# Optimization experiments

Hardware: AMD Instinct MI355X
Metric: run time of the kernel (lower is better)

The kernel has to match this reference:

```python
import jax, jax.numpy as jnp
import numpy as np
from jax import lax


def setup_inputs() -> dict:
    key = jax.random.key(0)
    k1, k2 = jax.random.split(key)
    B, H, W, Cin, Cout, kh, kw = 16, 128, 128, 128, 128, 3, 3
    X = jax.random.normal(k1, (B, H, W, Cin), dtype=jnp.float32)
    kernel = jax.random.normal(k2, (B, kh, kw, Cin, Cout), dtype=jnp.float32) * 0.05
    return {"X": X, "kernel": kernel}


def _conv_one(x, k):
    # x: [H, W, Cin]; k: [kh, kw, Cin, Cout] -> [H', W', Cout]
    out = lax.conv_general_dilated(
        x[None],  # [1, H, W, Cin]
        k,
        window_strides=(1, 1),
        padding='VALID',
        dimension_numbers=('NHWC', 'HWIO', 'NHWC'),
    )
    return out[0]


def reference(X, kernel):
    # Per-sample dynamic-filter conv: each batch element convolved with its own
    # [kh, kw, Cin, Cout] filter. Equivalent to the TF depthwise-reshape trick
    # followed by reduce_sum over the input-channel axis.
    return jax.vmap(_conv_one)(X, kernel)  # [B, H', W', Cout]
```

## Files before the change

### kernel.cpp

```cpp
#include <hip/hip_runtime.h>
#include <cstdint>

#define OWD 126
#define MTOT 15876

typedef short bf16x8 __attribute__((ext_vector_type(8)));
typedef float f32x4  __attribute__((ext_vector_type(4)));

#define BT_ELEMS  (16u * 128u * 1152u)
#define XBF_ELEMS (16u * 128u * 128u * 128u)
#define WS_NEEDED ((size_t)(BT_ELEMS + XBF_ELEMS) * 2)

__device__ __forceinline__ uint16_t f2bf(float f) {
    union { float f; uint32_t u; } v;
    v.f = f;
    uint32_t u = v.u;
    return (uint16_t)((u + 0x7FFFu + ((u >> 16) & 1u)) >> 16);
}

__device__ __forceinline__ uint32_t pk2(float a, float b) {
    return (uint32_t)f2bf(a) | ((uint32_t)f2bf(b) << 16);
}

__device__ __forceinline__ void gl_lds16(const uint16_t* g, uint16_t* l) {
    __builtin_amdgcn_global_load_lds(
        (const __attribute__((address_space(1))) uint32_t*)g,
        (__attribute__((address_space(3))) uint32_t*)l, 16, 0, 0);
}

__global__ __launch_bounds__(256) void kprep(const float* __restrict__ Kin,
                                             uint16_t* __restrict__ Bt) {
    const int rs = blockIdx.x;
    const int b  = blockIdx.y;
    const int t  = threadIdx.x;
    const int n  = t & 127;
    const int og = t >> 7;

    const float* src = Kin + (((size_t)b * 9 + rs) << 14);
    uint16_t*    dst = Bt + ((size_t)b * 128 + n) * 1152 + rs * 128;

#pragma unroll
    for (int o = 0; o < 8; ++o) {
        const int oct = og * 8 + o;
        const float* s0 = src + (oct * 8) * 128 + n;
        uint4 p;
        p.x = pk2(s0[0 * 128], s0[1 * 128]);
        p.y = pk2(s0[2 * 128], s0[3 * 128]);
        p.z = pk2(s0[4 * 128], s0[5 * 128]);
        p.w = pk2(s0[6 * 128], s0[7 * 128]);
        *(uint4*)(dst + oct * 8) = p;
    }
}

__global__ __launch_bounds__(256) void xprep(const float* __restrict__ X,
                                             uint16_t* __restrict__ Xbf) {
    const size_t i = ((size_t)blockIdx.x * 256 + threadIdx.x) * 8;
    const float4 a = *(const float4*)(X + i);
    const float4 b = *(const float4*)(X + i + 4);
    uint4 p;
    p.x = pk2(a.x, a.y);
    p.y = pk2(a.z, a.w);
    p.z = pk2(b.x, b.y);
    p.w = pk2(b.z, b.w);
    *(uint4*)(Xbf + i) = p;
}

__global__ __launch_bounds__(256) void conv_mfma_a(const uint16_t* __restrict__ Xbf,
                                                   const uint16_t* __restrict__ Bt,
                                                   float* __restrict__ Out) {
    __shared__ __align__(16) uint16_t lA[128 * 64];
    __shared__ __align__(16) uint16_t lB[128 * 64];

    const int mtile = blockIdx.x;
    const int b     = blockIdx.y;
    const int tid   = threadIdx.x;
    const int lane  = tid & 63;
    const int wave  = tid >> 6;
    const int wm    = (wave & 1) << 6;
    const int wn    = (wave >> 1) << 6;
    const int l15   = lane & 15;
    const int quad  = lane >> 4;

    const int kc = (lane & 7) ^ (lane >> 3);
    const uint16_t* Asrc[4];
    const uint16_t* Bsrc[4];
#pragma unroll
    for (int i = 0; i < 4; ++i) {
        const int row = wave * 32 + i * 8 + (lane >> 3);
        int m = mtile * 128 + row;
        if (m >= MTOT) m = MTOT - 1;
        const int oh = m / OWD, ow = m - oh * OWD;
        Asrc[i] = Xbf + (((size_t)b * 128 + oh) * 128 + ow) * 128 + kc * 8;
        Bsrc[i] = Bt + ((size_t)b * 128 + row) * 1152 + kc * 8;
    }
    uint16_t* Adst = &lA[(wave * 256 + lane) * 8];
    uint16_t* Bdst = &lB[(wave * 256 + lane) * 8];

    f32x4 acc[4][4];
#pragma unroll
    for (int i = 0; i < 4; ++i)
#pragma unroll
        for (int j = 0; j < 4; ++j)
            acc[i][j] = (f32x4){0.f, 0.f, 0.f, 0.f};

    for (int rs = 0; rs < 9; ++rs) {
        const int r = rs / 3;
        const int s = rs - r * 3;
        const int aoff = (r * 128 + s) * 128;
        const int boff = rs * 128;
#pragma unroll
        for (int half = 0; half < 2; ++half) {
            const int c0 = half * 64;

            __syncthreads();
#pragma unroll
            for (int i = 0; i < 4; ++i) {
                gl_lds16(Asrc[i] + aoff + c0, Adst + i * 512);
                gl_lds16(Bsrc[i] + boff + c0, Bdst + i * 512);
            }
            __syncthreads();

#pragma unroll
            for (int ksub = 0; ksub < 2; ++ksub) {
                bf16x8 af[4], bfr[4];
#pragma unroll
                for (int i = 0; i < 4; ++i) {
                    const int row = wm + i * 16 + l15;
                    const int pc  = (ksub * 4 + quad) ^ (row & 7);
                    af[i] = *(const bf16x8*)&lA[row * 64 + pc * 8];
                }
#pragma unroll
                for (int j = 0; j < 4; ++j) {
                    const int row = wn + j * 16 + l15;
                    const int pc  = (ksub * 4 + quad) ^ (row & 7);
                    bfr[j] = *(const bf16x8*)&lB[row * 64 + pc * 8];
                }
#pragma unroll
                for (int i = 0; i < 4; ++i)
#pragma unroll
                    for (int j = 0; j < 4; ++j)
                        acc[i][j] = __builtin_amdgcn_mfma_f32_16x16x32_bf16(
                            af[i], bfr[j], acc[i][j], 0, 0, 0);
            }
        }
    }

#pragma unroll
    for (int i = 0; i < 4; ++i) {
#pragma unroll
        for (int rr = 0; rr < 4; ++rr) {
            const int mrow = mtile * 128 + wm + i * 16 + quad * 4 + rr;
            if (mrow < MTOT) {
                const int oh2 = mrow / OWD;
                const int ow2 = mrow - oh2 * OWD;
                float* op = Out + (((size_t)b * OWD + oh2) * OWD + ow2) * 128 + wn + l15;
#pragma unroll
                for (int j = 0; j < 4; ++j)
                    op[j * 16] = acc[i][j][rr];
            }
        }
    }
}

__global__ __launch_bounds__(256) void conv_mfma(const float* __restrict__ X,
                                                 const uint16_t* __restrict__ Bt,
                                                 float* __restrict__ Out) {
    __shared__ __align__(16) uint16_t lA[128 * 64];
    __shared__ __align__(16) uint16_t lB[128 * 64];

    const int mtile = blockIdx.x;
    const int b     = blockIdx.y;
    const int tid   = threadIdx.x;
    const int lane  = tid & 63;
    const int wave  = tid >> 6;
    const int wm    = (wave & 1) << 6;
    const int wn    = (wave >> 1) << 6;
    const int l15   = lane & 15;
    const int quad  = lane >> 4;

    const int srow  = tid >> 1;
    const int shalf = tid & 1;

    int m = mtile * 128 + srow;
    if (m >= MTOT) m = MTOT - 1;
    const int oh = m / OWD;
    const int ow = m - oh * OWD;
    const float*    Xb = X + (((size_t)b * 128 + oh) * 128 + ow) * 128;
    const uint16_t* Bb = Bt + ((size_t)b * 128 + srow) * 1152 + shalf * 32;

    f32x4 acc[4][4];
#pragma unroll
    for (int i = 0; i < 4; ++i)
#pragma unroll
        for (int j = 0; j < 4; ++j)
            acc[i][j] = (f32x4){0.f, 0.f, 0.f, 0.f};

    for (int chunk = 0; chunk < 18; ++chunk) {
        const int rs = chunk >> 1;
        const int c0 = (chunk & 1) << 6;
        const int r  = rs / 3;
        const int s  = rs - r * 3;

        __syncthreads();
        {
            const float4* src = (const float4*)(Xb + (r * 128 + s) * 128 + c0 + shalf * 32);
            float4 v[8];
#pragma unroll
            for (int i = 0; i < 8; ++i) v[i] = src[i];
#pragma unroll
            for (int i = 0; i < 4; ++i) {
                uint4 p;
                p.x = pk2(v[2 * i].x, v[2 * i].y);
                p.y = pk2(v[2 * i].z, v[2 * i].w);
                p.z = pk2(v[2 * i + 1].x, v[2 * i + 1].y);
                p.w = pk2(v[2 * i + 1].z, v[2 * i + 1].w);
                const int ci = (shalf * 4 + i) ^ (srow & 7);
                *(uint4*)&lA[srow * 64 + ci * 8] = p;
            }
        }
        {
            const uint4* bsrc = (const uint4*)(Bb + rs * 128 + c0);
#pragma unroll
            for (int i = 0; i < 4; ++i) {
                const uint4 p = bsrc[i];
                const int ci = (shalf * 4 + i) ^ (srow & 7);
                *(uint4*)&lB[srow * 64 + ci * 8] = p;
            }
        }
        __syncthreads();

#pragma unroll
        for (int ksub = 0; ksub < 2; ++ksub) {
            bf16x8 af[4], bfr[4];
#pragma unroll
            for (int i = 0; i < 4; ++i) {
                const int row = wm + i * 16 + l15;
                const int ci  = (ksub * 4 + quad) ^ (row & 7);
                af[i] = *(const bf16x8*)&lA[row * 64 + ci * 8];
            }
#pragma unroll
            for (int j = 0; j < 4; ++j) {
                const int row = wn + j * 16 + l15;
                const int ci  = (ksub * 4 + quad) ^ (row & 7);
                bfr[j] = *(const bf16x8*)&lB[row * 64 + ci * 8];
            }
#pragma unroll
            for (int i = 0; i < 4; ++i)
#pragma unroll
                for (int j = 0; j < 4; ++j)
                    acc[i][j] = __builtin_amdgcn_mfma_f32_16x16x32_bf16(
                        af[i], bfr[j], acc[i][j], 0, 0, 0);
        }
    }

#pragma unroll
    for (int i = 0; i < 4; ++i) {
#pragma unroll
        for (int rr = 0; rr < 4; ++rr) {
            const int mrow = mtile * 128 + wm + i * 16 + quad * 4 + rr;
            if (mrow < MTOT) {
                const int oh2 = mrow / OWD;
                const int ow2 = mrow - oh2 * OWD;
                float* op = Out + (((size_t)b * OWD + oh2) * OWD + ow2) * 128 + wn + l15;
#pragma unroll
                for (int j = 0; j < 4; ++j)
                    op[j * 16] = acc[i][j][rr];
            }
        }
    }
}

extern "C" void kernel_launch(void* const* d_in, const int* in_sizes, int n_in,
                              void* d_out, int out_size, void* d_ws, size_t ws_size,
                              hipStream_t stream) {
    const float* X   = (const float*)d_in[0];
    const float* Kin = (const float*)d_in[1];
    float*       Out = (float*)d_out;
    uint16_t*    Bt  = (uint16_t*)d_ws;
    uint16_t*    Xbf = Bt + BT_ELEMS;

    kprep<<<dim3(9, 16), 256, 0, stream>>>(Kin, Bt);
    if (ws_size >= WS_NEEDED) {
        xprep<<<XBF_ELEMS / (256 * 8), 256, 0, stream>>>(X, Xbf);
        conv_mfma_a<<<dim3(125, 16), 256, 0, stream>>>(Xbf, Bt, Out);
    } else {
        conv_mfma<<<dim3(125, 16), 256, 0, stream>>>(X, Bt, Out);
    }
}
```

Baseline: 325.0 us.

## Double-buffer LDS tiles to overlap global loads with MFMA compute

Splits the shared-memory A and B tiles into two buffers and restructures the 18-step K loop so the next tile's global-to-LDS loads are issued before computing on the current buffer. This needs one barrier per step instead of two and lets memory latency hide behind MFMA work. It doubles LDS use to 64 KB per block, which may reduce occupancy. The row/column split is computed with a multiply-shift divide by three.

```diff
diff --git a/kernel.cpp b/kernel.cpp
--- a/kernel.cpp
+++ b/kernel.cpp
@@ -68,8 +68,8 @@
 __global__ __launch_bounds__(256) void conv_mfma_a(const uint16_t* __restrict__ Xbf,
                                                    const uint16_t* __restrict__ Bt,
                                                    float* __restrict__ Out) {
-    __shared__ __align__(16) uint16_t lA[128 * 64];
-    __shared__ __align__(16) uint16_t lB[128 * 64];
+    __shared__ __align__(16) uint16_t lA[2][128 * 64];
+    __shared__ __align__(16) uint16_t lB[2][128 * 64];
 
     const int mtile = blockIdx.x;
     const int b     = blockIdx.y;
@@ -93,8 +93,7 @@
         Asrc[i] = Xbf + (((size_t)b * 128 + oh) * 128 + ow) * 128 + kc * 8;
         Bsrc[i] = Bt + ((size_t)b * 128 + row) * 1152 + kc * 8;
     }
-    uint16_t* Adst = &lA[(wave * 256 + lane) * 8];
-    uint16_t* Bdst = &lB[(wave * 256 + lane) * 8];
+    const int dbase = (wave * 256 + lane) * 8;
 
     f32x4 acc[4][4];
 #pragma unroll
@@ -103,47 +102,68 @@
         for (int j = 0; j < 4; ++j)
             acc[i][j] = (f32x4){0.f, 0.f, 0.f, 0.f};
 
-    for (int rs = 0; rs < 9; ++rs) {
-        const int r = rs / 3;
-        const int s = rs - r * 3;
-        const int aoff = (r * 128 + s) * 128;
-        const int boff = rs * 128;
-#pragma unroll
-        for (int half = 0; half < 2; ++half) {
-            const int c0 = half * 64;
-
-            __syncthreads();
-#pragma unroll
-            for (int i = 0; i < 4; ++i) {
-                gl_lds16(Asrc[i] + aoff + c0, Adst + i * 512);
-                gl_lds16(Bsrc[i] + boff + c0, Bdst + i * 512);
-            }
-            __syncthreads();
-
-#pragma unroll
-            for (int ksub = 0; ksub < 2; ++ksub) {
-                bf16x8 af[4], bfr[4];
-#pragma unroll
-                for (int i = 0; i < 4; ++i) {
-                    const int row = wm + i * 16 + l15;
-                    const int pc  = (ksub * 4 + quad) ^ (row & 7);
-                    af[i] = *(const bf16x8*)&lA[row * 64 + pc * 8];
-                }
-#pragma unroll
-                for (int j = 0; j < 4; ++j) {
-                    const int row = wn + j * 16 + l15;
-                    const int pc  = (ksub * 4 + quad) ^ (row & 7);
-                    bfr[j] = *(const bf16x8*)&lB[row * 64 + pc * 8];
-                }
-#pragma unroll
-                for (int i = 0; i < 4; ++i)
-#pragma unroll
-                    for (int j = 0; j < 4; ++j)
-                        acc[i][j] = __builtin_amdgcn_mfma_f32_16x16x32_bf16(
-                            af[i], bfr[j], acc[i][j], 0, 0, 0);
-            }
-        }
-    }
+#define STAGE(t_, bu_)                                                      \
+    {                                                                       \
+        const int rs_ = (t_) >> 1;                                         \
+        const int c0_ = ((t_) & 1) << 6;                                   \
+        const int r_  = (rs_ * 11) >> 5;                \
+        const int s_  = rs_ - r_ * 3;                                      \
+        const int ao_ = (r_ * 128 + s_) * 128 + c0_;                       \
+        const int bo_ = rs_ * 128 + c0_;                                   \
+        uint16_t* Ad_ = &lA[bu_][dbase];                                   \
+        uint16_t* Bd_ = &lB[bu_][dbase];                                   \
+        _Pragma("unroll")                                                  \
+        for (int i_ = 0; i_ < 4; ++i_) {                                   \
+            gl_lds16(Asrc[i_] + ao_, Ad_ + i_ * 512);                      \
+            gl_lds16(Bsrc[i_] + bo_, Bd_ + i_ * 512);                      \
+        }                                                                  \
+    }
+
+#define COMPUTE(bu_)                                                        \
+    {                                                                       \
+        _Pragma("unroll")                                                  \
+        for (int ksub_ = 0; ksub_ < 2; ++ksub_) {                          \
+            bf16x8 af[4], bfr[4];                                          \
+            _Pragma("unroll")                                              \
+            for (int i_ = 0; i_ < 4; ++i_) {                               \
+                const int row_ = wm + i_ * 16 + l15;                       \
+                const int pc_  = (ksub_ * 4 + quad) ^ (row_ & 7);          \
+                af[i_] = *(const bf16x8*)&lA[bu_][row_ * 64 + pc_ * 8];    \
+            }                                                              \
+            _Pragma("unroll")                                              \
+            for (int j_ = 0; j_ < 4; ++j_) {                               \
+                const int row_ = wn + j_ * 16 + l15;                       \
+                const int pc_  = (ksub_ * 4 + quad) ^ (row_ & 7);          \
+                bfr[j_] = *(const bf16x8*)&lB[bu_][row_ * 64 + pc_ * 8];   \
+            }                                                              \
+            _Pragma("unroll")                                              \
+            for (int i_ = 0; i_ < 4; ++i_)                                 \
+                _Pragma("unroll")                                          \
+                for (int j_ = 0; j_ < 4; ++j_)                             \
+                    acc[i_][j_] = __builtin_amdgcn_mfma_f32_16x16x32_bf16( \
+                        af[i_], bfr[j_], acc[i_][j_], 0, 0, 0);            \
+        }                                                                  \
+    }
+
+    STAGE(0, 0);
+    __syncthreads();
+
+#pragma unroll 1
+    for (int t = 0; t < 16; t += 2) {
+        STAGE(t + 1, 1);
+        COMPUTE(0);
+        __syncthreads();
+        STAGE(t + 2, 0);
+        COMPUTE(1);
+        __syncthreads();
+    }
+    STAGE(17, 1);
+    COMPUTE(0);
+    __syncthreads();
+    COMPUTE(1);
+
+#undef STAGE
+#undef COMPUTE
 
 #pragma unroll
     for (int i = 0; i < 4; ++i) {
```

New measurement: 324.6 us. No clear change (-0.1%).
